# Performance work log

Measured on AMD Instinct MI355X. Metric: run time of the kernel, lower is better.

The kernel has to match this reference:

```python
import jax, jax.numpy as jnp
import numpy as np

B, T = 2, 512
D, H, DFF = 1024, 16, 4096
V, CSL = 32000, 16
NL, NDL = 4, 2
MAXLEN = 1024
DH = D // H


def generate_ar_mask(L, csl):
    m = np.zeros((2 * L, 2 * L), dtype=bool)
    for i in range(L):
        m[:i] = True
        m[L + (i // csl) * csl: L + i] = True
    return jnp.asarray(m)


def generate_block_ntp_mask(L, csl):
    m = np.zeros((2 * L, 2 * L), dtype=bool)
    for c in range(L // csl):
        if c - 1 >= 0:
            m[:(c - 1) * csl] = True
        m[L + c * csl: L + (c + 1) * csl] = True
    return jnp.asarray(m)


def layernorm(x, g, b, eps=1e-5):
    mu = x.mean(-1, keepdims=True)
    var = x.var(-1, keepdims=True)
    return (x - mu) / jnp.sqrt(var + eps) * g + b


def block(x, mask, p):
    ln1g, ln1b, wqkv, bqkv, wo, bo, ln2g, ln2b, w1, b1, w2, b2 = p
    h = layernorm(x, ln1g, ln1b)
    qkv = h @ wqkv + bqkv                       # [B,S,3D]
    q, k, v = jnp.split(qkv, 3, axis=-1)
    bs, S, _ = x.shape
    q = q.reshape(bs, S, H, DH).transpose(0, 2, 1, 3)
    k = k.reshape(bs, S, H, DH).transpose(0, 2, 1, 3)
    v = v.reshape(bs, S, H, DH).transpose(0, 2, 1, 3)
    scores = jnp.einsum('bhqd,bhkd->bhqk', q, k) / jnp.sqrt(jnp.asarray(DH, x.dtype))
    scores = jnp.where(mask, scores, jnp.asarray(-1e9, x.dtype))
    attn = jax.nn.softmax(scores, axis=-1)
    o = jnp.einsum('bhqk,bhkd->bhqd', attn, v)
    o = o.transpose(0, 2, 1, 3).reshape(bs, S, D)
    x = x + (o @ wo + bo)
    h = layernorm(x, ln2g, ln2b)
    return x + (jax.nn.gelu(h @ w1 + b1, approximate=False) @ w2 + b2)


def setup_inputs():
    key = jax.random.key(0)
    ks = jax.random.split(key, 6)

    def pstack(k, n):
        kk = jax.random.split(k, 4)
        return dict(
            ln1g=jnp.ones((n, D)), ln1b=jnp.zeros((n, D)),
            wqkv=0.02 * jax.random.normal(kk[0], (n, D, 3 * D)), bqkv=jnp.zeros((n, 3 * D)),
            wo=0.02 * jax.random.normal(kk[1], (n, D, D)), bo=jnp.zeros((n, D)),
            ln2g=jnp.ones((n, D)), ln2b=jnp.zeros((n, D)),
            w1=0.02 * jax.random.normal(kk[2], (n, D, DFF)), b1=jnp.zeros((n, DFF)),
            w2=0.02 * jax.random.normal(kk[3], (n, DFF, D)), b2=jnp.zeros((n, D)))

    body = pstack(ks[0], NL)
    dec = pstack(ks[1], NDL)
    inp = {
        'tok_ids': jax.random.randint(ks[2], (B, T), 0, V),
        'tok_emb': 0.02 * jax.random.normal(ks[3], (V, D)),
        'pos_emb': 0.02 * jax.random.normal(ks[4], (MAXLEN, D)),
        'mask_tokens': 0.02 * jax.random.normal(ks[5], (1, CSL, D)),
    }
    for kname, vv in body.items():
        inp['b_' + kname] = vv
    for kname, vv in dec.items():
        inp['d_' + kname] = vv
    return inp


def reference(tok_ids, tok_emb, pos_emb, mask_tokens,
              b_ln1g, b_ln1b, b_wqkv, b_bqkv, b_wo, b_bo, b_ln2g, b_ln2b, b_w1, b_b1, b_w2, b_b2,
              d_ln1g, d_ln1b, d_wqkv, d_bqkv, d_wo, d_bo, d_ln2g, d_ln2b, d_w1, d_b1, d_w2, d_b2):
    Bq, Tq = tok_ids.shape
    pos = jnp.tile(jnp.arange(Tq), 2)            # pos ids repeated for both halves
    emb_pos = pos_emb[pos]                       # [2T, D], broadcast over batch
    mask_ids = jnp.tile(mask_tokens, (Bq, Tq // CSL, 1))
    x = jnp.concatenate([tok_emb[tok_ids], mask_ids], axis=1) + emb_pos[None]

    body_mask = generate_block_ntp_mask(Tq, CSL)
    bp = (b_ln1g, b_ln1b, b_wqkv, b_bqkv, b_wo, b_bo, b_ln2g, b_ln2b, b_w1, b_b1, b_w2, b_b2)
    for i in range(NL):
        x = block(x, body_mask, tuple(p[i] for p in bp))

    ar_mask = generate_ar_mask(Tq, CSL)
    dp = (d_ln1g, d_ln1b, d_wqkv, d_bqkv, d_wo, d_bo, d_ln2g, d_ln2b, d_w1, d_b1, d_w2, d_b2)
    for i in range(NDL):
        x = block(x, ar_mask, tuple(p[i] for p in dp))

    logits = (x @ tok_emb.T)[:, Tq + 1:, :]      # [B, T-1, V]
    tgt = tok_ids[:, :-1].reshape(-1)
    logits = logits.reshape(-1, V)
    logp = jax.nn.log_softmax(logits, axis=-1)
    loss = -jnp.take_along_axis(logp, tgt[:, None], axis=1).mean()
    return loss
```

## Files before the change

### kernel.cpp

```cpp
#include <hip/hip_runtime.h>
#include <hip/hip_bf16.h>
#include <math.h>

#define DD   1024
#define HHN  16
#define DHD  64
#define DFFN 4096
#define VV   32000
#define BBN  2
#define TTN  512
#define SSN  1024
#define NRN  2048

typedef __attribute__((ext_vector_type(8))) short short8;
typedef __attribute__((ext_vector_type(4))) float f32x4;

enum : long {
    LSTR    = 12582912,
    OFF_QKV = 0,
    OFF_WO  = 3145728,
    OFF_W1  = 4194304,
    OFF_W2  = 8388608
};

struct P24 { const float* p[24]; };

__device__ __forceinline__ unsigned short f2bf(float f) {
    __hip_bfloat16 h = __float2bfloat16(f);
    return __builtin_bit_cast(unsigned short, h);
}
__device__ __forceinline__ float bf2f(unsigned short u) {
    return __bfloat162float(__builtin_bit_cast(__hip_bfloat16, u));
}

__device__ __forceinline__ void glds16(const void* g, void* l) {
    __builtin_amdgcn_global_load_lds(
        (const __attribute__((address_space(1))) void*)g,
        (__attribute__((address_space(3))) void*)l,
        16, 0, 0);
}

__device__ __forceinline__ float blockReduceSum(float v) {
    __shared__ float sh[4];
    #pragma unroll
    for (int o = 1; o < 64; o <<= 1) v += __shfl_xor(v, o, 64);
    int lane = threadIdx.x & 63, wv = threadIdx.x >> 6;
    __syncthreads();
    if (lane == 0) sh[wv] = v;
    __syncthreads();
    return sh[0] + sh[1] + sh[2] + sh[3];
}

__global__ __launch_bounds__(256) void prep_k(P24 wp, unsigned short* __restrict__ wbf,
                                              const int* __restrict__ tok,
                                              const float* __restrict__ temb,
                                              const float* __restrict__ pemb,
                                              const float* __restrict__ mtok,
                                              float* __restrict__ x) {
    __shared__ __align__(16) float Lf[64][68];
    const int id = blockIdx.x;
    const int t = threadIdx.x;

    if (id < 18432) {
        int seg, base, K, N;
        long woff;
        if (id < 4608)       { seg = 0; base = 0;     K = DD;   N = 3 * DD; woff = OFF_QKV; }
        else if (id < 6144)  { seg = 1; base = 4608;  K = DD;   N = DD;     woff = OFF_WO;  }
        else if (id < 12288) { seg = 2; base = 6144;  K = DD;   N = DFFN;   woff = OFF_W1;  }
        else                 { seg = 3; base = 12288; K = DFFN; N = DD;     woff = OFF_W2;  }
        const int rid = id - base;
        const int tpl = (K / 64) * (N / 64);
        const int lz = rid / tpl, t2 = rid % tpl;
        const int nt = N / 64;
        const int n0 = (t2 % nt) * 64, k0 = (t2 / nt) * 64;
        const float* w = wp.p[seg * 6 + lz];
        unsigned short* wt = wbf + (size_t)lz * LSTR + woff;

        {
            const int kr = t >> 2, nc = (t & 3) * 16;
            const float* src = w + (size_t)(k0 + kr) * N + n0 + nc;
            float4 f0 = ((const float4*)src)[0];
            float4 f1 = ((const float4*)src)[1];
            float4 f2 = ((const float4*)src)[2];
            float4 f3 = ((const float4*)src)[3];
            *(float4*)&Lf[kr][nc]      = f0;
            *(float4*)&Lf[kr][nc + 4]  = f1;
            *(float4*)&Lf[kr][nc + 8]  = f2;
            *(float4*)&Lf[kr][nc + 12] = f3;
        }
        __syncthreads();
        {
            const int nr = t & 63, kc = (t >> 6) * 16;
            __align__(16) unsigned short tmp[16];
            #pragma unroll
            for (int i = 0; i < 16; i++) tmp[i] = f2bf(Lf[kc + i][nr]);
            unsigned short* d2 = wt + (size_t)(n0 + nr) * K + k0 + kc;
            *(int4*)d2       = *(const int4*)&tmp[0];
            *(int4*)(d2 + 8) = *(const int4*)&tmp[8];
        }
    } else {
        const int row = id - 18432;
        const int b = row >> 10, s = row & 1023;
        const int d = t * 4;
        const float* src;
        const float* pe;
        if (s < TTN) {
            int tid2 = tok[b * TTN + s];
            src = temb + (size_t)tid2 * DD + d;
            pe  = pemb + (size_t)s * DD + d;
        } else {
            int sm = s - TTN;
            src = mtok + (size_t)(sm & 15) * DD + d;
            pe  = pemb + (size_t)sm * DD + d;
        }
        float4 v = *(const float4*)src;
        float4 p = *(const float4*)pe;
        v.x += p.x; v.y += p.y; v.z += p.z; v.w += p.w;
        *(float4*)(x + (size_t)row * DD + d) = v;
    }
}

__global__ __launch_bounds__(256) void ln_k(const float* __restrict__ x,
                                            const float* __restrict__ g,
                                            const float* __restrict__ b,
                                            unsigned short* __restrict__ out) {
    int row = blockIdx.x;
    int d = threadIdx.x * 4;
    const float4 v = *(const float4*)(x + (size_t)row * DD + d);
    float s  = v.x + v.y + v.z + v.w;
    float ss = v.x * v.x + v.y * v.y + v.z * v.z + v.w * v.w;
    s  = blockReduceSum(s);
    ss = blockReduceSum(ss);
    float mu  = s * (1.0f / DD);
    float var = ss * (1.0f / DD) - mu * mu;
    float inv = rsqrtf(var + 1e-5f);
    const float4 gg = *(const float4*)(g + d);
    const float4 bb = *(const float4*)(b + d);
    ushort4 o;
    o.x = f2bf((v.x - mu) * inv * gg.x + bb.x);
    o.y = f2bf((v.y - mu) * inv * gg.y + bb.y);
    o.z = f2bf((v.z - mu) * inv * gg.z + bb.z);
    o.w = f2bf((v.w - mu) * inv * gg.w + bb.w);
    *(ushort4*)(out + (size_t)row * DD + d) = o;
}

__global__ __launch_bounds__(256) void conv_k(const float* __restrict__ w,
                                              unsigned short* __restrict__ o, long n) {
    long i = ((long)blockIdx.x * 256 + threadIdx.x) * 8;
    if (i >= n) return;
    float4 a = *(const float4*)(w + i);
    float4 b = *(const float4*)(w + i + 4);
    __align__(16) unsigned short tmp[8];
    tmp[0] = f2bf(a.x); tmp[1] = f2bf(a.y); tmp[2] = f2bf(a.z); tmp[3] = f2bf(a.w);
    tmp[4] = f2bf(b.x); tmp[5] = f2bf(b.y); tmp[6] = f2bf(b.z); tmp[7] = f2bf(b.w);
    *(int4*)(o + i) = *(const int4*)tmp;
}

__global__ __launch_bounds__(256, 2) void flash_k(
    const unsigned short* __restrict__ qkvb,
    unsigned short* __restrict__ o,
    int mtype) {
    __shared__ __align__(16) unsigned short Qs[128][72];
    __shared__ __align__(16) unsigned short Ks[64][72];
    __shared__ __align__(16) unsigned short Vs[64][72];
    __shared__ __align__(16) unsigned short Ps[128][72];
    __shared__ float vcol[64];

    const int blk = blockIdx.x;
    const int bh = blk >> 3, qt = blk & 7;
    const int b = bh >> 4, h = bh & 15;
    const int t = threadIdx.x;
    const int lane = t & 63;
    const int w = t >> 6;
    const int fr = lane & 15;
    const int g8 = (lane >> 4) * 8;
    const int g4 = (lane >> 4) * 4;

    {
        const int r = t >> 1, c0 = (t & 1) * 32;
        const unsigned short* src =
            qkvb + (size_t)(b * SSN + qt * 128 + r) * 3072 + h * 64 + c0;
        *(int4*)&Qs[r][c0]      = *(const int4*)(src);
        *(int4*)&Qs[r][c0 + 8]  = *(const int4*)(src + 8);
        *(int4*)&Qs[r][c0 + 16] = *(const int4*)(src + 16);
        *(int4*)&Qs[r][c0 + 24] = *(const int4*)(src + 24);
    }
    __syncthreads();
    short8 aq[2][2];
    #pragma unroll
    for (int m = 0; m < 2; m++)
        #pragma unroll
        for (int kk = 0; kk < 2; kk++)
            aq[m][kk] = *(const short8*)&Qs[w * 32 + m * 16 + fr][kk * 32 + g8];

    float mrun[2][4], lrun[2][4];
    f32x4 accO[2][4] = {};
    #pragma unroll
    for (int m = 0; m < 2; m++)
        #pragma unroll
        for (int j = 0; j < 4; j++) { mrun[m][j] = -1e30f; lrun[m][j] = 0.f; }

    float vacc[16];
    #pragma unroll
    for (int j = 0; j < 16; j++) vacc[j] = 0.f;

    const unsigned short* kbase = qkvb + (size_t)(b * SSN) * 3072 + DD + h * 64;
    const unsigned short* vbase = qkvb + (size_t)(b * SSN) * 3072 + 2 * DD + h * 64;
    const int d0 = w * 16;

    for (int kt = 0; kt < 16; kt++) {
        __syncthreads();
        {
            const int r = t >> 2, c0 = (t & 3) * 16;
            const unsigned short* src = kbase + (size_t)(kt * 64 + r) * 3072 + c0;
            *(int4*)&Ks[r][c0]     = *(const int4*)(src);
            *(int4*)&Ks[r][c0 + 8] = *(const int4*)(src + 8);
        }
        {
            const unsigned short* src = vbase + (size_t)(kt * 64 + lane) * 3072 + d0;
            int4 q0 = *(const int4*)(src);
            int4 q1 = *(const int4*)(src + 8);
            const unsigned short* u = (const unsigned short*)&q0;
            #pragma unroll
            for (int j = 0; j < 8; j++) {
                Vs[d0 + j][lane] = u[j];
                vacc[j] += bf2f(u[j]);
            }
            const unsigned short* u2 = (const unsigned short*)&q1;
            #pragma unroll
            for (int j = 0; j < 8; j++) {
                Vs[d0 + 8 + j][lane] = u2[j];
                vacc[8 + j] += bf2f(u2[j]);
            }
        }
        __syncthreads();

        short8 bk[4][2];
        #pragma unroll
        for (int n = 0; n < 4; n++)
            #pragma unroll
            for (int kk = 0; kk < 2; kk++)
                bk[n][kk] = *(const short8*)&Ks[n * 16 + fr][kk * 32 + g8];

        #pragma unroll
        for (int m = 0; m < 2; m++) {
            f32x4 a2[4] = {};
            #pragma unroll
            for (int n = 0; n < 4; n++) {
                a2[n] = __builtin_amdgcn_mfma_f32_16x16x32_bf16(aq[m][0], bk[n][0], a2[n], 0, 0, 0);
                a2[n] = __builtin_amdgcn_mfma_f32_16x16x32_bf16(aq[m][1], bk[n][1], a2[n], 0, 0, 0);
            }
            #pragma unroll
            for (int j = 0; j < 4; j++) {
                float tm = fmaxf(fmaxf(a2[0][j], a2[1][j]), fmaxf(a2[2][j], a2[3][j]));
                tm *= 0.125f;
                #pragma unroll
                for (int o2 = 1; o2 < 16; o2 <<= 1) tm = fmaxf(tm, __shfl_xor(tm, o2, 64));
                const float mn = fmaxf(mrun[m][j], tm);
                const float alpha = __expf(mrun[m][j] - mn);
                mrun[m][j] = mn;
                float rs = 0.f;
                #pragma unroll
                for (int n = 0; n < 4; n++) {
                    float pv = __expf(a2[n][j] * 0.125f - mn);
                    rs += pv;
                    Ps[w * 32 + m * 16 + g4 + j][n * 16 + fr] = f2bf(pv);
                }
                #pragma unroll
                for (int o2 = 1; o2 < 16; o2 <<= 1) rs += __shfl_xor(rs, o2, 64);
                lrun[m][j] = lrun[m][j] * alpha + rs;
                #pragma unroll
                for (int nd = 0; nd < 4; nd++) accO[m][nd][j] *= alpha;
            }
        }
        #pragma unroll
        for (int kk = 0; kk < 2; kk++) {
            short8 pa0 = *(const short8*)&Ps[w * 32 + fr][kk * 32 + g8];
            short8 pa1 = *(const short8*)&Ps[w * 32 + 16 + fr][kk * 32 + g8];
            #pragma unroll
            for (int nd = 0; nd < 4; nd++) {
                short8 vb = *(const short8*)&Vs[nd * 16 + fr][kk * 32 + g8];
                accO[0][nd] = __builtin_amdgcn_mfma_f32_16x16x32_bf16(pa0, vb, accO[0][nd], 0, 0, 0);
                accO[1][nd] = __builtin_amdgcn_mfma_f32_16x16x32_bf16(pa1, vb, accO[1][nd], 0, 0, 0);
            }
        }
    }

    #pragma unroll
    for (int j = 0; j < 16; j++) {
        float vs = vacc[j];
        #pragma unroll
        for (int o2 = 1; o2 < 64; o2 <<= 1) vs += __shfl_xor(vs, o2, 64);
        if (lane == j) vcol[d0 + j] = vs;
    }
    __syncthreads();

    #pragma unroll
    for (int m = 0; m < 2; m++)
        #pragma unroll
        for (int nd = 0; nd < 4; nd++)
            #pragma unroll
            for (int j = 0; j < 4; j++) {
                const int row = qt * 128 + w * 32 + m * 16 + g4 + j;
                const int col = nd * 16 + fr;
                bool uni;
                if (mtype == 0) uni = (row >= 480 && row < 512);
                else            uni = (row == 511) || (row >= 512 && (row & 15) == 15);
                float val;
                if (uni) val = vcol[col] * (1.0f / 1024.0f);
                else     val = accO[m][nd][j] / lrun[m][j];
                o[(size_t)(b * SSN + row) * DD + h * 64 + col] = f2bf(val);
            }
}

template <bool DOLN>
__global__ __launch_bounds__(256) void rln_k(const float* __restrict__ pp,
                                             const float* __restrict__ bias,
                                             float* __restrict__ x,
                                             const float* __restrict__ g,
                                             const float* __restrict__ b,
                                             unsigned short* __restrict__ xb) {
    const int row = blockIdx.x;
    const int d = threadIdx.x * 4;
    const size_t off = (size_t)row * DD + d;
    float4 v = *(const float4*)(x + off);
    #pragma unroll
    for (int sl = 0; sl < 4; sl++) {
        float4 p = *(const float4*)(pp + (size_t)sl * NRN * DD + off);
        v.x += p.x; v.y += p.y; v.z += p.z; v.w += p.w;
    }
    const float4 bv = *(const float4*)(bias + d);
    v.x += bv.x; v.y += bv.y; v.z += bv.z; v.w += bv.w;
    *(float4*)(x + off) = v;
    if (DOLN) {
        float s  = v.x + v.y + v.z + v.w;
        float ss = v.x * v.x + v.y * v.y + v.z * v.z + v.w * v.w;
        s  = blockReduceSum(s);
        ss = blockReduceSum(ss);
        float mu  = s * (1.0f / DD);
        float var = ss * (1.0f / DD) - mu * mu;
        float inv = rsqrtf(var + 1e-5f);
        const float4 gg = *(const float4*)(g + d);
        const float4 bb = *(const float4*)(b + d);
        ushort4 ov;
        ov.x = f2bf((v.x - mu) * inv * gg.x + bb.x);
        ov.y = f2bf((v.y - mu) * inv * gg.y + bb.y);
        ov.z = f2bf((v.z - mu) * inv * gg.z + bb.z);
        ov.w = f2bf((v.w - mu) * inv * gg.w + bb.w);
        *(ushort4*)(xb + off) = ov;
    }
}

__global__ __launch_bounds__(256) void gather_xl_k(const float* __restrict__ x,
                                                   unsigned short* __restrict__ xl) {
    int r = blockIdx.x;
    int d = threadIdx.x * 4;
    ushort4 o = {0, 0, 0, 0};
    if (r < 1022) {
        int b = r / 511, i = r % 511;
        float4 v = *(const float4*)(x + (size_t)(b * SSN + 513 + i) * DD + d);
        o.x = f2bf(v.x); o.y = f2bf(v.y); o.z = f2bf(v.z); o.w = f2bf(v.w);
    }
    *(ushort4*)(xl + (size_t)r * DD + d) = o;
}

__global__ __launch_bounds__(256) void loss_row2_k(const float2* __restrict__ part,
                                                   const float* __restrict__ tgtlog,
                                                   float* __restrict__ rowloss) {
    const int r = blockIdx.x;
    const int t = threadIdx.x;
    float mx = -1e30f, s = 0.f;
    for (int i = t; i < 500; i += 256) {
        float2 p = part[(size_t)r * 500 + i];
        float m2 = fmaxf(mx, p.x);
        s = s * __expf(mx - m2) + p.y * __expf(p.x - m2);
        mx = m2;
    }
    #pragma unroll
    for (int o2 = 1; o2 < 64; o2 <<= 1) {
        float om = __shfl_xor(mx, o2, 64);
        float os = __shfl_xor(s, o2, 64);
        float m2 = fmaxf(mx, om);
        s = s * __expf(mx - m2) + os * __expf(om - m2);
        mx = m2;
    }
    __shared__ float shm[4], shs[4];
    int lane = t & 63, wv = t >> 6;
    if (lane == 0) { shm[wv] = mx; shs[wv] = s; }
    __syncthreads();
    if (t == 0) {
        float M = fmaxf(fmaxf(shm[0], shm[1]), fmaxf(shm[2], shm[3]));
        float S = shs[0] * __expf(shm[0] - M) + shs[1] * __expf(shm[1] - M)
                + shs[2] * __expf(shm[2] - M) + shs[3] * __expf(shm[3] - M);
        rowloss[r] = (logf(S) + M) - tgtlog[r];
    }
}

__global__ __launch_bounds__(256) void loss_final_k(const float* __restrict__ rowloss,
                                                    float* __restrict__ out) {
    int t = threadIdx.x;
    float s = 0.f;
    for (int i = t; i < 1022; i += 256) s += rowloss[i];
    s = blockReduceSum(s);
    if (t == 0) out[0] = s * (1.0f / 1022.0f);
}

template <int EPI, int KSPLIT>
__global__ __launch_bounds__(256) void gemm_k(
    const unsigned short* __restrict__ A, long lda,
    const unsigned short* __restrict__ Bt, long ldb,
    void* __restrict__ Cp, long ldc,
    const float* __restrict__ bias,
    int MT, int K, long kstr) {
    __shared__ __align__(16) unsigned short As[2][128][32];
    __shared__ __align__(16) unsigned short Bs[2][128][32];

    const int nwg = gridDim.x;
    const int q = nwg >> 3, r = nwg & 7;
    const int xcd = blockIdx.x & 7, lin = blockIdx.x >> 3;
    const int wg = (xcd < r ? xcd * (q + 1) : r * (q + 1) + (xcd - r) * q) + lin;
    const int tiles = nwg / KSPLIT;
    const int ks = wg / tiles;
    const int rem = wg % tiles;
    const int brow = (rem % MT) * 128;
    const int bcol = (rem / MT) * 128;
    const int Kl = K / KSPLIT;

    const int t = threadIdx.x;
    const int lane = t & 63;
    const int w = t >> 6;
    const int fr = lane & 15;
    const int g8 = (lane >> 4) * 8;

    const int sr = w * 32 + (lane >> 2);
    const int sc = (lane & 3) * 8;
    const unsigned short* aP0 = A + (size_t)(brow + sr) * lda + ks * Kl + sc;
    const unsigned short* aP1 = aP0 + (size_t)16 * lda;
    const unsigned short* bP0 = Bt + (size_t)(bcol + sr) * ldb + ks * Kl + sc;
    const unsigned short* bP1 = bP0 + (size_t)16 * ldb;

    f32x4 acc[4][4] = {};
    const int nsteps = Kl >> 5;

    glds16(aP0, &As[0][w * 32][0]);
    glds16(aP1, &As[0][w * 32 + 16][0]);
    glds16(bP0, &Bs[0][w * 32][0]);
    glds16(bP1, &Bs[0][w * 32 + 16][0]);
    aP0 += 32; aP1 += 32; bP0 += 32; bP1 += 32;
    asm volatile("s_waitcnt vmcnt(0)");
    __syncthreads();

    int cur = 0;
    for (int s2 = 1; s2 < nsteps; ++s2) {
        const int nb = cur ^ 1;
        glds16(aP0, &As[nb][w * 32][0]);
        glds16(aP1, &As[nb][w * 32 + 16][0]);
        glds16(bP0, &Bs[nb][w * 32][0]);
        glds16(bP1, &Bs[nb][w * 32 + 16][0]);
        aP0 += 32; aP1 += 32; bP0 += 32; bP1 += 32;

        short8 af[4], bf[4];
        #pragma unroll
        for (int m = 0; m < 4; m++)
            af[m] = *(const short8*)&As[cur][(w >> 1) * 64 + m * 16 + fr][g8];
        #pragma unroll
        for (int n = 0; n < 4; n++)
            bf[n] = *(const short8*)&Bs[cur][(w & 1) * 64 + n * 16 + fr][g8];
        #pragma unroll
        for (int m = 0; m < 4; m++)
            #pragma unroll
            for (int n = 0; n < 4; n++)
                acc[m][n] = __builtin_amdgcn_mfma_f32_16x16x32_bf16(af[m], bf[n], acc[m][n], 0, 0, 0);
        __syncthreads();
        cur = nb;
    }
    {
        short8 af[4], bf[4];
        #pragma unroll
        for (int m = 0; m < 4; m++)
            af[m] = *(const short8*)&As[cur][(w >> 1) * 64 + m * 16 + fr][g8];
        #pragma unroll
        for (int n = 0; n < 4; n++)
            bf[n] = *(const short8*)&Bs[cur][(w & 1) * 64 + n * 16 + fr][g8];
        #pragma unroll
        for (int m = 0; m < 4; m++)
            #pragma unroll
            for (int n = 0; n < 4; n++)
                acc[m][n] = __builtin_amdgcn_mfma_f32_16x16x32_bf16(af[m], bf[n], acc[m][n], 0, 0, 0);
    }

    const int wr = (w >> 1) * 64;
    const int wc = (w & 1) * 64;
    const int g4 = (lane >> 4) * 4;
    #pragma unroll
    for (int n = 0; n < 4; n++) {
        const int col = bcol + wc + n * 16 + fr;
        const float bv = bias ? bias[col] : 0.f;
        #pragma unroll
        for (int m = 0; m < 4; m++) {
            #pragma unroll
            for (int j = 0; j < 4; j++) {
                const int row = brow + wr + m * 16 + g4 + j;
                float v = acc[m][n][j] + bv;
                const size_t ci = (size_t)row * ldc + col;
                if (EPI == 0) {
                    ((float*)Cp)[ci] = v;
                } else if (EPI == 1) {
                    ((unsigned short*)Cp)[ci] = f2bf(v);
                } else if (EPI == 2) {
                    float gl = 0.5f * v * (1.0f + erff(v * 0.70710678118654752f));
                    ((unsigned short*)Cp)[ci] = f2bf(gl);
                } else if (EPI == 3) {
                    ((float*)Cp)[ci] += v;
                } else {
                    ((float*)Cp)[(size_t)ks * kstr + ci] = v;
                }
            }
        }
    }
}

__global__ __launch_bounds__(256) void gemm_lse_k(
    const unsigned short* __restrict__ A,
    const unsigned short* __restrict__ Bt,
    float2* __restrict__ part,
    float* __restrict__ tgtlog,
    const int* __restrict__ tok) {
    __shared__ __align__(16) unsigned short As[2][128][32];
    __shared__ __align__(16) unsigned short Bs[2][128][32];

    const int nwg = gridDim.x;
    const int q = nwg >> 3, r = nwg & 7;
    const int xcd = blockIdx.x & 7, lin = blockIdx.x >> 3;
    const int wg = (xcd < r ? xcd * (q + 1) : r * (q + 1) + (xcd - r) * q) + lin;
    const int MT = 8;
    const int brow = (wg % MT) * 128;
    const int bcol = (wg / MT) * 128;

    const int t = threadIdx.x;
    const int lane = t & 63;
    const int w = t >> 6;
    const int fr = lane & 15;
    const int g8 = (lane >> 4) * 8;

    const int sr = w * 32 + (lane >> 2);
    const int sc = (lane & 3) * 8;
    const unsigned short* aP0 = A + (size_t)(brow + sr) * DD + sc;
    const unsigned short* aP1 = aP0 + (size_t)16 * DD;
    const unsigned short* bP0 = Bt + (size_t)(bcol + sr) * DD + sc;
    const unsigned short* bP1 = bP0 + (size_t)16 * DD;

    f32x4 acc[4][4] = {};

    glds16(aP0, &As[0][w * 32][0]);
    glds16(aP1, &As[0][w * 32 + 16][0]);
    glds16(bP0, &Bs[0][w * 32][0]);
    glds16(bP1, &Bs[0][w * 32 + 16][0]);
    aP0 += 32; aP1 += 32; bP0 += 32; bP1 += 32;
    asm volatile("s_waitcnt vmcnt(0)");
    __syncthreads();

    int cur = 0;
    for (int s2 = 1; s2 < 32; ++s2) {
        const int nb = cur ^ 1;
        glds16(aP0, &As[nb][w * 32][0]);
        glds16(aP1, &As[nb][w * 32 + 16][0]);
        glds16(bP0, &Bs[nb][w * 32][0]);
        glds16(bP1, &Bs[nb][w * 32 + 16][0]);
        aP0 += 32; aP1 += 32; bP0 += 32; bP1 += 32;

        short8 af[4], bf[4];
        #pragma unroll
        for (int m = 0; m < 4; m++)
            af[m] = *(const short8*)&As[cur][(w >> 1) * 64 + m * 16 + fr][g8];
        #pragma unroll
        for (int n = 0; n < 4; n++)
            bf[n] = *(const short8*)&Bs[cur][(w & 1) * 64 + n * 16 + fr][g8];
        #pragma unroll
        for (int m = 0; m < 4; m++)
            #pragma unroll
            for (int n = 0; n < 4; n++)
                acc[m][n] = __builtin_amdgcn_mfma_f32_16x16x32_bf16(af[m], bf[n], acc[m][n], 0, 0, 0);
        __syncthreads();
        cur = nb;
    }
    {
        short8 af[4], bf[4];
        #pragma unroll
        for (int m = 0; m < 4; m++)
            af[m] = *(const short8*)&As[cur][(w >> 1) * 64 + m * 16 + fr][g8];
        #pragma unroll
        for (int n = 0; n < 4; n++)
            bf[n] = *(const short8*)&Bs[cur][(w & 1) * 64 + n * 16 + fr][g8];
        #pragma unroll
        for (int m = 0; m < 4; m++)
            #pragma unroll
            for (int n = 0; n < 4; n++)
                acc[m][n] = __builtin_amdgcn_mfma_f32_16x16x32_bf16(af[m], bf[n], acc[m][n], 0, 0, 0);
    }

    const int wr = (w >> 1) * 64;
    const int wc = (w & 1) * 64;
    const int g4 = (lane >> 4) * 4;
    const int ct2 = (bcol >> 7) * 2 + (w & 1);
    #pragma unroll
    for (int m = 0; m < 4; m++) {
        #pragma unroll
        for (int j = 0; j < 4; j++) {
            const int grow = brow + wr + m * 16 + g4 + j;
            const float v0 = acc[m][0][j], v1 = acc[m][1][j];
            const float v2 = acc[m][2][j], v3 = acc[m][3][j];
            float mx = fmaxf(fmaxf(v0, v1), fmaxf(v2, v3));
            #pragma unroll
            for (int o2 = 1; o2 < 16; o2 <<= 1) mx = fmaxf(mx, __shfl_xor(mx, o2, 64));
            float s = __expf(v0 - mx) + __expf(v1 - mx) + __expf(v2 - mx) + __expf(v3 - mx);
            #pragma unroll
            for (int o2 = 1; o2 < 16; o2 <<= 1) s += __shfl_xor(s, o2, 64);
            if (fr == 0) {
                float2 p; p.x = mx; p.y = s;
                part[(size_t)grow * 500 + ct2] = p;
            }
            int tgtc = -1;
            if (grow < 511) tgtc = tok[grow];
            else if (grow >= 511 && grow < 1022) tgtc = tok[512 + grow - 511];
            const int cl = tgtc - (bcol + wc);
            if (tgtc >= 0 && cl >= 0 && cl < 64 && (cl & 15) == fr) {
                const float vv[4] = {v0, v1, v2, v3};
                tgtlog[grow] = vv[cl >> 4];
            }
        }
    }
}

extern "C" void kernel_launch(void* const* d_in, const int* in_sizes, int n_in,
                              void* d_out, int out_size, void* d_ws, size_t ws_size,
                              hipStream_t stream) {
    const int*   tok  = (const int*)d_in[0];
    const float* temb = (const float*)d_in[1];
    const float* pemb = (const float*)d_in[2];
    const float* mtok = (const float*)d_in[3];
    const float* W[24];
    for (int i = 0; i < 24; i++) W[i] = (const float*)d_in[4 + i];

    char* ws = (char*)d_ws;
    float*          x      = (float*)(ws + 0);
    unsigned short* xb     = (unsigned short*)(ws + 8388608);
    unsigned short* qkvb   = (unsigned short*)(ws + 12582912);
    unsigned short* o      = (unsigned short*)(ws + 25165824);
    unsigned short* g      = (unsigned short*)(ws + 29360128);
    float*          pp     = (float*)(ws + 46137344);
    unsigned short* wbf    = (unsigned short*)(ws + 79691776);
    unsigned short* tembb  = (unsigned short*)(ws + 79691776);
    float2*         part   = (float2*)(ws + 145227776);
    float*          tgtlog = (float*)(ws + 149327872);
    unsigned short* xl     = (unsigned short*)(ws + 230686720);
    float*          rowloss= (float*)(ws + 232783872);

    P24 wp;
    for (int l = 0; l < 6; l++) {
        const int grp = (l < 4) ? 0 : 1;
        const int li  = (l < 4) ? l : l - 4;
        const float* const* P = W + grp * 12;
        wp.p[0 + l]  = P[2]  + (size_t)li * DD * 3 * DD;
        wp.p[6 + l]  = P[4]  + (size_t)li * DD * DD;
        wp.p[12 + l] = P[8]  + (size_t)li * DD * DFFN;
        wp.p[18 + l] = P[10] + (size_t)li * DFFN * DD;
    }
    prep_k<<<18432 + 2048, 256, 0, stream>>>(wp, wbf, tok, temb, pemb, mtok, x);

    for (int l = 0; l < 6; l++) {
        const int grp = (l < 4) ? 0 : 1;
        const int li  = (l < 4) ? l : l - 4;
        const float* const* P = W + grp * 12;
        const float* ln1g = P[0] + (size_t)li * DD;
        const float* ln1b = P[1] + (size_t)li * DD;
        const float* bqkv = P[3] + (size_t)li * 3 * DD;
        const float* bo   = P[5] + (size_t)li * DD;
        const float* ln2g = P[6] + (size_t)li * DD;
        const float* ln2b = P[7] + (size_t)li * DD;
        const float* b1   = P[9] + (size_t)li * DFFN;
        const float* b2   = P[11] + (size_t)li * DD;
        unsigned short* wl = wbf + (size_t)l * LSTR;

        if (l == 0) ln_k<<<NRN, 256, 0, stream>>>(x, ln1g, ln1b, xb);
        gemm_k<1, 1><<<16 * 24, 256, 0, stream>>>(xb, DD, wl + OFF_QKV, DD,
                                                  qkvb, 3 * DD, bqkv, 16, DD, 0);
        flash_k<<<256, 256, 0, stream>>>(qkvb, o, grp);
        gemm_k<3, 1><<<16 * 8, 256, 0, stream>>>(o, DD, wl + OFF_WO, DD,
                                                 x, DD, bo, 16, DD, 0);

        ln_k<<<NRN, 256, 0, stream>>>(x, ln2g, ln2b, xb);
        gemm_k<2, 1><<<16 * 32, 256, 0, stream>>>(xb, DD, wl + OFF_W1, DD,
                                                  g, DFFN, b1, 16, DD, 0);
        gemm_k<4, 4><<<16 * 8 * 4, 256, 0, stream>>>(g, DFFN, wl + OFF_W2, DFFN,
                                                     pp, DD, nullptr, 16, DFFN,
                                                     (long)NRN * DD);
        if (l < 5) {
            const int l2 = l + 1;
            const int grp2 = (l2 < 4) ? 0 : 1;
            const int li2  = (l2 < 4) ? l2 : l2 - 4;
            const float* const* P2 = W + grp2 * 12;
            rln_k<true><<<NRN, 256, 0, stream>>>(pp, b2, x,
                                                 P2[0] + (size_t)li2 * DD,
                                                 P2[1] + (size_t)li2 * DD, xb);
        } else {
            rln_k<false><<<NRN, 256, 0, stream>>>(pp, b2, x, nullptr, nullptr, nullptr);
        }
    }

    gather_xl_k<<<1024, 256, 0, stream>>>(x, xl);
    conv_k<<<16000, 256, 0, stream>>>(temb, tembb, (long)VV * DD);
    gemm_lse_k<<<2000, 256, 0, stream>>>(xl, tembb, part, tgtlog, tok);
    loss_row2_k<<<1022, 256, 0, stream>>>(part, tgtlog, rowloss);
    loss_final_k<<<1, 256, 0, stream>>>(rowloss, (float*)d_out);
}
```

Measured before the change: 1.501 ms.

## Fuse bf16 conversion of embeddings into LSE GEMM and merge gather into residual kernel

Removes the separate conv_k pass over the vocabulary embedding: gemm_lse_k now loads fp32 embedding rows, converts them to bf16 in registers and stores them to LDS after the MFMA step. The final-row gather kernel is folded into the last rln_k, which writes the bf16 logits-input rows directly. The weight-prep kernel is retiled to 256×64 tiles, converting to bf16 before the LDS transpose. The aim is fewer launches and less HBM round-tripping, at the cost of redundant conversion across row tiles and synchronous B loads in the GEMM.

```diff
diff --git a/kernel.cpp b/kernel.cpp
--- a/kernel.cpp
+++ b/kernel.cpp
@@ -57,49 +57,54 @@
                                               const float* __restrict__ pemb,
                                               const float* __restrict__ mtok,
                                               float* __restrict__ x) {
-    __shared__ __align__(16) float Lf[64][68];
+    __shared__ __align__(16) unsigned short Lb[256][72];
     const int id = blockIdx.x;
     const int t = threadIdx.x;
 
-    if (id < 18432) {
+    if (id < 4608) {
         int seg, base, K, N;
         long woff;
-        if (id < 4608)       { seg = 0; base = 0;     K = DD;   N = 3 * DD; woff = OFF_QKV; }
-        else if (id < 6144)  { seg = 1; base = 4608;  K = DD;   N = DD;     woff = OFF_WO;  }
-        else if (id < 12288) { seg = 2; base = 6144;  K = DD;   N = DFFN;   woff = OFF_W1;  }
-        else                 { seg = 3; base = 12288; K = DFFN; N = DD;     woff = OFF_W2;  }
+        if (id < 1152)      { seg = 0; base = 0;    K = DD;   N = 3 * DD; woff = OFF_QKV; }
+        else if (id < 1536) { seg = 1; base = 1152; K = DD;   N = DD;     woff = OFF_WO;  }
+        else if (id < 3072) { seg = 2; base = 1536; K = DD;   N = DFFN;   woff = OFF_W1;  }
+        else                { seg = 3; base = 3072; K = DFFN; N = DD;     woff = OFF_W2;  }
         const int rid = id - base;
-        const int tpl = (K / 64) * (N / 64);
+        const int tpl = (K / 256) * (N / 64);
         const int lz = rid / tpl, t2 = rid % tpl;
         const int nt = N / 64;
-        const int n0 = (t2 % nt) * 64, k0 = (t2 / nt) * 64;
+        const int n0 = (t2 % nt) * 64, k0 = (t2 / nt) * 256;
         const float* w = wp.p[seg * 6 + lz];
         unsigned short* wt = wbf + (size_t)lz * LSTR + woff;
 
-        {
-            const int kr = t >> 2, nc = (t & 3) * 16;
-            const float* src = w + (size_t)(k0 + kr) * N + n0 + nc;
-            float4 f0 = ((const float4*)src)[0];
-            float4 f1 = ((const float4*)src)[1];
-            float4 f2 = ((const float4*)src)[2];
-            float4 f3 = ((const float4*)src)[3];
-            *(float4*)&Lf[kr][nc]      = f0;
-            *(float4*)&Lf[kr][nc + 4]  = f1;
-            *(float4*)&Lf[kr][nc + 8]  = f2;
-            *(float4*)&Lf[kr][nc + 12] = f3;
+        #pragma unroll
+        for (int p = 0; p < 2; p++) {
+            const int k = p * 128 + (t >> 1);
+            const int nch = (t & 1) * 32;
+            const float* src = w + (size_t)(k0 + k) * N + n0 + nch;
+            __align__(16) unsigned short tmp[32];
+            #pragma unroll
+            for (int i = 0; i < 8; i++) {
+                float4 f = ((const float4*)src)[i];
+                tmp[i * 4 + 0] = f2bf(f.x); tmp[i * 4 + 1] = f2bf(f.y);
+                tmp[i * 4 + 2] = f2bf(f.z); tmp[i * 4 + 3] = f2bf(f.w);
+            }
+            #pragma unroll
+            for (int i = 0; i < 4; i++)
+                *(int4*)&Lb[k][nch + i * 8] = *(const int4*)&tmp[i * 8];
         }
         __syncthreads();
         {
-            const int nr = t & 63, kc = (t >> 6) * 16;
-            __align__(16) unsigned short tmp[16];
-            #pragma unroll
-            for (int i = 0; i < 16; i++) tmp[i] = f2bf(Lf[kc + i][nr]);
-            unsigned short* d2 = wt + (size_t)(n0 + nr) * K + k0 + kc;
-            *(int4*)d2       = *(const int4*)&tmp[0];
-            *(int4*)(d2 + 8) = *(const int4*)&tmp[8];
+            const int row = t >> 2, kc = (t & 3) * 64;
+            __align__(16) unsigned short tmp[64];
+            #pragma unroll
+            for (int i = 0; i < 64; i++) tmp[i] = Lb[kc + i][row];
+            unsigned short* dst = wt + (size_t)(n0 + row) * K + k0 + kc;
+            #pragma unroll
+            for (int i = 0; i < 8; i++)
+                *(int4*)(dst + i * 8) = *(const int4*)&tmp[i * 8];
         }
     } else {
-        const int row = id - 18432;
+        const int row = id - 4608;
         const int b = row >> 10, s = row & 1023;
         const int d = t * 4;
         const float* src;
@@ -144,18 +149,6 @@
     *(ushort4*)(out + (size_t)row * DD + d) = o;
 }
 
-__global__ __launch_bounds__(256) void conv_k(const float* __restrict__ w,
-                                              unsigned short* __restrict__ o, long n) {
-    long i = ((long)blockIdx.x * 256 + threadIdx.x) * 8;
-    if (i >= n) return;
-    float4 a = *(const float4*)(w + i);
-    float4 b = *(const float4*)(w + i + 4);
-    __align__(16) unsigned short tmp[8];
-    tmp[0] = f2bf(a.x); tmp[1] = f2bf(a.y); tmp[2] = f2bf(a.z); tmp[3] = f2bf(a.w);
-    tmp[4] = f2bf(b.x); tmp[5] = f2bf(b.y); tmp[6] = f2bf(b.z); tmp[7] = f2bf(b.w);
-    *(int4*)(o + i) = *(const int4*)tmp;
-}
-
 __global__ __launch_bounds__(256, 2) void flash_k(
     const unsigned short* __restrict__ qkvb,
     unsigned short* __restrict__ o,
@@ -319,7 +312,8 @@
                                              float* __restrict__ x,
                                              const float* __restrict__ g,
                                              const float* __restrict__ b,
-                                             unsigned short* __restrict__ xb) {
+                                             unsigned short* __restrict__ xb,
+                                             unsigned short* __restrict__ xl) {
     const int row = blockIdx.x;
     const int d = threadIdx.x * 4;
     const size_t off = (size_t)row * DD + d;
@@ -348,20 +342,15 @@
         ov.z = f2bf((v.z - mu) * inv * gg.z + bb.z);
         ov.w = f2bf((v.w - mu) * inv * gg.w + bb.w);
         *(ushort4*)(xb + off) = ov;
-    }
-}
-
-__global__ __launch_bounds__(256) void gather_xl_k(const float* __restrict__ x,
-                                                   unsigned short* __restrict__ xl) {
-    int r = blockIdx.x;
-    int d = threadIdx.x * 4;
-    ushort4 o = {0, 0, 0, 0};
-    if (r < 1022) {
-        int b = r / 511, i = r % 511;
-        float4 v = *(const float4*)(x + (size_t)(b * SSN + 513 + i) * DD + d);
-        o.x = f2bf(v.x); o.y = f2bf(v.y); o.z = f2bf(v.z); o.w = f2bf(v.w);
-    }
-    *(ushort4*)(xl + (size_t)r * DD + d) = o;
+    } else {
+        const int s = row & 1023;
+        if (s >= 513) {
+            const int xr = (row >> 10) * 511 + (s - 513);
+            ushort4 ov;
+            ov.x = f2bf(v.x); ov.y = f2bf(v.y); ov.z = f2bf(v.z); ov.w = f2bf(v.w);
+            *(ushort4*)(xl + (size_t)xr * DD + d) = ov;
+        }
+    }
 }
 
 __global__ __launch_bounds__(256) void loss_row2_k(const float2* __restrict__ part,
@@ -522,12 +511,12 @@
 
 __global__ __launch_bounds__(256) void gemm_lse_k(
     const unsigned short* __restrict__ A,
-    const unsigned short* __restrict__ Bt,
+    const float* __restrict__ Btf,
     float2* __restrict__ part,
     float* __restrict__ tgtlog,
     const int* __restrict__ tok) {
     __shared__ __align__(16) unsigned short As[2][128][32];
-    __shared__ __align__(16) unsigned short Bs[2][128][32];
+    __shared__ __align__(16) unsigned short Bs[2][128][40];
 
     const int nwg = gridDim.x;
     const int q = nwg >> 3, r = nwg & 7;
@@ -543,31 +532,45 @@
     const int fr = lane & 15;
     const int g8 = (lane >> 4) * 8;
 
-    const int sr = w * 32 + (lane >> 2);
-    const int sc = (lane & 3) * 8;
-    const unsigned short* aP0 = A + (size_t)(brow + sr) * DD + sc;
+    const int sra = w * 32 + (lane >> 2);
+    const int sca = (lane & 3) * 8;
+    const unsigned short* aP0 = A + (size_t)(brow + sra) * DD + sca;
     const unsigned short* aP1 = aP0 + (size_t)16 * DD;
-    const unsigned short* bP0 = Bt + (size_t)(bcol + sr) * DD + sc;
-    const unsigned short* bP1 = bP0 + (size_t)16 * DD;
+    const int rb = w * 32 + (lane >> 1);
+    const int kb = (lane & 1) * 16;
+    const float* bP = Btf + (size_t)(bcol + rb) * DD + kb;
 
     f32x4 acc[4][4] = {};
 
     glds16(aP0, &As[0][w * 32][0]);
     glds16(aP1, &As[0][w * 32 + 16][0]);
-    glds16(bP0, &Bs[0][w * 32][0]);
-    glds16(bP1, &Bs[0][w * 32 + 16][0]);
-    aP0 += 32; aP1 += 32; bP0 += 32; bP1 += 32;
+    aP0 += 32; aP1 += 32;
+    {
+        __align__(16) unsigned short tmp[16];
+        #pragma unroll
+        for (int i = 0; i < 4; i++) {
+            float4 f = ((const float4*)bP)[i];
+            tmp[i * 4 + 0] = f2bf(f.x); tmp[i * 4 + 1] = f2bf(f.y);
+            tmp[i * 4 + 2] = f2bf(f.z); tmp[i * 4 + 3] = f2bf(f.w);
+        }
+        *(int4*)&Bs[0][rb][kb]     = *(const int4*)&tmp[0];
+        *(int4*)&Bs[0][rb][kb + 8] = *(const int4*)&tmp[8];
+    }
+    bP += 32;
     asm volatile("s_waitcnt vmcnt(0)");
     __syncthreads();
 
     int cur = 0;
     for (int s2 = 1; s2 < 32; ++s2) {
         const int nb = cur ^ 1;
+        float4 f0 = ((const float4*)bP)[0];
+        float4 f1 = ((const float4*)bP)[1];
+        float4 f2 = ((const float4*)bP)[2];
+        float4 f3 = ((const float4*)bP)[3];
+        bP += 32;
         glds16(aP0, &As[nb][w * 32][0]);
         glds16(aP1, &As[nb][w * 32 + 16][0]);
-        glds16(bP0, &Bs[nb][w * 32][0]);
-        glds16(bP1, &Bs[nb][w * 32 + 16][0]);
-        aP0 += 32; aP1 += 32; bP0 += 32; bP1 += 32;
+        aP0 += 32; aP1 += 32;
 
         short8 af[4], bf[4];
         #pragma unroll
@@ -581,6 +584,16 @@
             #pragma unroll
             for (int n = 0; n < 4; n++)
                 acc[m][n] = __builtin_amdgcn_mfma_f32_16x16x32_bf16(af[m], bf[n], acc[m][n], 0, 0, 0);
+
+        {
+            __align__(16) unsigned short tmp[16];
+            tmp[0] = f2bf(f0.x); tmp[1] = f2bf(f0.y); tmp[2]  = f2bf(f0.z); tmp[3]  = f2bf(f0.w);
+            tmp[4] = f2bf(f1.x); tmp[5] = f2bf(f1.y); tmp[6]  = f2bf(f1.z); tmp[7]  = f2bf(f1.w);
+            tmp[8] = f2bf(f2.x); tmp[9] = f2bf(f2.y); tmp[10] = f2bf(f2.z); tmp[11] = f2bf(f2.w);
+            tmp[12] = f2bf(f3.x); tmp[13] = f2bf(f3.y); tmp[14] = f2bf(f3.z); tmp[15] = f2bf(f3.w);
+            *(int4*)&Bs[nb][rb][kb]     = *(const int4*)&tmp[0];
+            *(int4*)&Bs[nb][rb][kb + 8] = *(const int4*)&tmp[8];
+        }
         __syncthreads();
         cur = nb;
     }
@@ -650,7 +663,6 @@
     unsigned short* g      = (unsigned short*)(ws + 29360128);
     float*          pp     = (float*)(ws + 46137344);
     unsigned short* wbf    = (unsigned short*)(ws + 79691776);
-    unsigned short* tembb  = (unsigned short*)(ws + 79691776);
     float2*         part   = (float2*)(ws + 145227776);
     float*          tgtlog = (float*)(ws + 149327872);
     unsigned short* xl     = (unsigned short*)(ws + 230686720);
@@ -666,7 +678,7 @@
         wp.p[12 + l] = P[8]  + (size_t)li * DD * DFFN;
         wp.p[18 + l] = P[10] + (size_t)li * DFFN * DD;
     }
-    prep_k<<<18432 + 2048, 256, 0, stream>>>(wp, wbf, tok, temb, pemb, mtok, x);
+    prep_k<<<4608 + 2048, 256, 0, stream>>>(wp, wbf, tok, temb, pemb, mtok, x);
 
     for (int l = 0; l < 6; l++) {
         const int grp = (l < 4) ? 0 : 1;
@@ -702,15 +714,13 @@
             const float* const* P2 = W + grp2 * 12;
             rln_k<true><<<NRN, 256, 0, stream>>>(pp, b2, x,
                                                  P2[0] + (size_t)li2 * DD,
-                                                 P2[1] + (size_t)li2 * DD, xb);
+                                                 P2[1] + (size_t)li2 * DD, xb, nullptr);
         } else {
-            rln_k<false><<<NRN, 256, 0, stream>>>(pp, b2, x, nullptr, nullptr, nullptr);
-        }
-    }
-
-    gather_xl_k<<<1024, 256, 0, stream>>>(x, xl);
-    conv_k<<<16000, 256, 0, stream>>>(temb, tembb, (long)VV * DD);
-    gemm_lse_k<<<2000, 256, 0, stream>>>(xl, tembb, part, tgtlog, tok);
+            rln_k<false><<<NRN, 256, 0, stream>>>(pp, b2, x, nullptr, nullptr, nullptr, xl);
+        }
+    }
+
+    gemm_lse_k<<<2000, 256, 0, stream>>>(xl, temb, part, tgtlog, tok);
     loss_row2_k<<<1022, 256, 0, stream>>>(part, tgtlog, rowloss);
     loss_final_k<<<1, 256, 0, stream>>>(rowloss, (float*)d_out);
 }
```

Result: slower. 1.578 ms (+5.1%).
